# Kernel tuning notes

Measured on AMD Instinct MI355X. Metric: run time of the kernel, lower is better.

## Reference

```python
import jax, jax.numpy as jnp
import numpy as np

DIM = 2048
H = 16       # num_heads
HKV = 4      # num_kv_heads
HD = DIM // H  # head_dim = 128
REP = H // HKV
ROPE_BASE = 10000.0
QK_GAIN_INIT = 1.0
B, T = 4, 2048


def rms_norm(x):
    # F.rms_norm with eps=None -> machine eps of dtype, no weight
    eps = jnp.finfo(x.dtype).eps
    return x * jax.lax.rsqrt(jnp.mean(x * x, axis=-1, keepdims=True) + eps)


def apply_rotary_emb(x, cos, sin):
    # x: [B, h, T, HD]; cos/sin: [T, HD//2]
    h = x.shape[-1] // 2
    x1, x2 = x[..., :h], x[..., h:]
    return jnp.concatenate((x1 * cos + x2 * sin, -x1 * sin + x2 * cos), axis=-1)


def setup_inputs() -> dict:
    key = jax.random.key(0)
    ks = jax.random.split(key, 6)
    kv_dim = HKV * HD
    x = jax.random.normal(ks[0], (B, T, DIM), dtype=jnp.float32)
    Wq = jax.random.normal(ks[1], (DIM, DIM), dtype=jnp.float32) * 0.02
    Wk = jax.random.normal(ks[2], (kv_dim, DIM), dtype=jnp.float32) * 0.02
    Wv = jax.random.normal(ks[3], (kv_dim, DIM), dtype=jnp.float32) * 0.02
    Wproj = jax.random.normal(ks[4], (DIM, DIM), dtype=jnp.float32) * 0.02
    q_gain = jnp.full((H,), QK_GAIN_INIT, dtype=jnp.float32)
    return {"x": x, "Wq": Wq, "Wk": Wk, "Wv": Wv, "Wproj": Wproj, "q_gain": q_gain}


def reference(x, Wq, Wk, Wv, Wproj, q_gain):
    Bs, Ts, D = x.shape
    # QKV projections (bias-free Linear: x @ W.T)
    q = (x @ Wq.T).reshape(Bs, Ts, H, HD).transpose(0, 2, 1, 3)      # [B,H,T,HD]
    k = (x @ Wk.T).reshape(Bs, Ts, HKV, HD).transpose(0, 2, 1, 3)    # [B,HKV,T,HD]
    v = (x @ Wv.T).reshape(Bs, Ts, HKV, HD).transpose(0, 2, 1, 3)
    # RMSNorm over head_dim
    q, k = rms_norm(q), rms_norm(k)
    # rotary
    inv_freq = 1.0 / (ROPE_BASE ** (jnp.arange(0, HD, 2, dtype=jnp.float32) / HD))
    t = jnp.arange(Ts, dtype=jnp.float32)
    freqs = jnp.outer(t, inv_freq)  # [T, HD//2]
    cos, sin = jnp.cos(freqs), jnp.sin(freqs)
    q = apply_rotary_emb(q, cos, sin)
    k = apply_rotary_emb(k, cos, sin)
    # per-head query gain
    q = q * q_gain[None, :, None, None]
    # GQA attention without materializing repeated K/V
    qg = q.reshape(Bs, HKV, REP, Ts, HD)
    scale = 1.0 / jnp.sqrt(jnp.asarray(HD, dtype=q.dtype))
    scores = jnp.einsum('bgrtd,bgsd->bgrts', qg, k) * scale  # [B,HKV,REP,T,T]
    causal = jnp.tril(jnp.ones((Ts, Ts), dtype=bool))
    scores = jnp.where(causal, scores, jnp.finfo(scores.dtype).min)
    attn = jax.nn.softmax(scores, axis=-1)
    y = jnp.einsum('bgrts,bgsd->bgrtd', attn, v)              # [B,HKV,REP,T,HD]
    y = y.reshape(Bs, H, Ts, HD).transpose(0, 2, 1, 3).reshape(Bs, Ts, D)
    return y @ Wproj.T
```

## Files before the change

### kernel.cpp

```cpp
#include <hip/hip_runtime.h>
#include <stdint.h>

typedef unsigned short u16;
typedef __attribute__((ext_vector_type(4))) float f32x4;
typedef __attribute__((ext_vector_type(8))) __bf16 bf16x8;
typedef __attribute__((ext_vector_type(4))) u16 u16x4;
typedef __attribute__((ext_vector_type(8))) u16 u16x8;

#define T_SEQ 2048
#define NB 4
#define NH 16
#define NKV 4
#define HDIM 128
#define PSTR 72

__device__ __forceinline__ u16 f2bf(float f) {
  __bf16 h = (__bf16)f;
  return __builtin_bit_cast(u16, h);
}
__device__ __forceinline__ float bf2f(u16 u) {
  union { uint32_t u; float f; } v; v.u = ((uint32_t)u) << 16;
  return v.f;
}
__device__ __forceinline__ void gload16(const void* g, void* l) {
  __builtin_amdgcn_global_load_lds((const __attribute__((address_space(1))) void*)g,
                                   (__attribute__((address_space(3))) void*)l, 16, 0, 0);
}
__device__ __forceinline__ f32x4 mfma16(bf16x8 a, bf16x8 b, f32x4 c) {
  return __builtin_amdgcn_mfma_f32_16x16x32_bf16(a, b, c, 0, 0, 0);
}

__global__ __launch_bounds__(256) void cvt_all(const float* __restrict__ x,
                                               const float* __restrict__ wq,
                                               const float* __restrict__ wk,
                                               const float* __restrict__ wv,
                                               const float* __restrict__ wp,
                                               u16* __restrict__ xo, u16* __restrict__ wqo,
                                               u16* __restrict__ wko, u16* __restrict__ wvo,
                                               u16* __restrict__ wpo) {
  const int C_X = 16777216 / 4, C_WQ = 4194304 / 4, C_WKV = 1048576 / 4;
  const int B1 = C_X, B2 = B1 + C_WQ, B3 = B2 + C_WKV, B4 = B3 + C_WKV;
  const int total = B4 + C_WQ;
  int idx = blockIdx.x * 256 + threadIdx.x;
  int stride = gridDim.x * 256;
  for (int c = idx; c < total; c += stride) {
    const float* src;
    u16* dst;
    int off;
    if (c < B1)      { src = x;  dst = xo;  off = c; }
    else if (c < B2) { src = wq; dst = wqo; off = c - B1; }
    else if (c < B3) { src = wk; dst = wko; off = c - B2; }
    else if (c < B4) { src = wv; dst = wvo; off = c - B3; }
    else             { src = wp; dst = wpo; off = c - B4; }
    f32x4 v = *(const f32x4*)(src + (size_t)off * 4);
    u16x4 o;
    o[0] = f2bf(v[0]); o[1] = f2bf(v[1]); o[2] = f2bf(v[2]); o[3] = f2bf(v[3]);
    *(u16x4*)(dst + (size_t)off * 4) = o;
  }
}

template <int MODE>
__global__ __launch_bounds__(256) void gemm128p3(const u16* __restrict__ A,
                                                 const u16* __restrict__ Bt,
                                                 u16* __restrict__ k_o, u16* __restrict__ v_o,
                                                 float* __restrict__ f_o,
                                                 int K, int nx, int cpx) {
  __shared__ __align__(16) u16 As3[3 * 128 * 32];
  __shared__ __align__(16) u16 Bs3[3 * 128 * 32];
  const int tid = threadIdx.x;
  const int l = tid & 63, w = tid >> 6;
  const int l15 = l & 15, g16 = l >> 4;
  const int wr = w >> 1, wc = w & 1;

  const int oid = blockIdx.x + nx * blockIdx.y;
  const int wid = (oid & 7) * cpx + (oid >> 3);
  const int m0 = (wid / nx) * 128, n0 = (wid % nx) * 128;

  f32x4 acc[4][4] = {};

  const int row0 = tid >> 2, row1 = 64 + (tid >> 2), cc = tid & 3;
  const int sc0 = cc ^ ((row0 >> 1) & 3), sc1 = cc ^ ((row1 >> 1) & 3);
  const u16* pA0 = A + (size_t)(m0 + row0) * K + sc0 * 8;
  const u16* pA1 = A + (size_t)(m0 + row1) * K + sc1 * 8;
  const u16* pB0 = Bt + (size_t)(n0 + row0) * K + sc0 * 8;
  const u16* pB1 = Bt + (size_t)(n0 + row1) * K + sc1 * 8;

#define STAGE(buf)                                                   \
  {                                                                  \
    char* ab = (char*)As3 + (buf) * 8192 + w * 1024;                 \
    char* bb = (char*)Bs3 + (buf) * 8192 + w * 1024;                 \
    gload16(pA0, ab);                                                \
    gload16(pA1, ab + 4096);                                         \
    gload16(pB0, bb);                                                \
    gload16(pB1, bb + 4096);                                         \
    pA0 += 32; pA1 += 32; pB0 += 32; pB1 += 32;                      \
  }

#define COMPUTE(buf)                                                 \
  {                                                                  \
    const u16* AsB = As3 + (buf) * 4096;                             \
    const u16* BsB = Bs3 + (buf) * 4096;                             \
    bf16x8 af[4], bfr[4];                                            \
    _Pragma("unroll")                                                \
    for (int mt = 0; mt < 4; ++mt) {                                 \
      int arow = wr * 64 + mt * 16 + l15;                            \
      af[mt] = *(const bf16x8*)&AsB[arow * 32 +                      \
                                    ((g16 ^ ((arow >> 1) & 3)) * 8)];\
    }                                                                \
    _Pragma("unroll")                                                \
    for (int nt = 0; nt < 4; ++nt) {                                 \
      int brow = wc * 64 + nt * 16 + l15;                            \
      bfr[nt] = *(const bf16x8*)&BsB[brow * 32 +                     \
                                     ((g16 ^ ((brow >> 1) & 3)) * 8)];\
    }                                                                \
    __builtin_amdgcn_s_setprio(1);                                   \
    _Pragma("unroll")                                                \
    for (int mt = 0; mt < 4; ++mt)                                   \
      _Pragma("unroll")                                              \
      for (int nt = 0; nt < 4; ++nt)                                 \
        acc[mt][nt] = mfma16(af[mt], bfr[nt], acc[mt][nt]);          \
    __builtin_amdgcn_s_setprio(0);                                   \
  }

  const int ntiles = K >> 5;
  STAGE(0);
  STAGE(1);
  asm volatile("s_waitcnt vmcnt(4)" ::: "memory");
  __builtin_amdgcn_s_barrier();

  int cur = 0, nxt = 2;
  for (int t = 0; t < ntiles; ++t) {
    const bool more2 = (t + 2 < ntiles);
    if (more2) STAGE(nxt);
    COMPUTE(cur);
    if (t + 1 < ntiles) {
      if (more2) {
        asm volatile("s_waitcnt vmcnt(4)" ::: "memory");
      } else {
        asm volatile("s_waitcnt vmcnt(0)" ::: "memory");
      }
      __builtin_amdgcn_s_barrier();
    }
    cur = (cur == 2) ? 0 : cur + 1;
    nxt = (nxt == 2) ? 0 : nxt + 1;
  }
#undef STAGE
#undef COMPUTE

#pragma unroll
  for (int mt = 0; mt < 4; ++mt) {
#pragma unroll
    for (int r = 0; r < 4; ++r) {
      int row = m0 + wr * 64 + mt * 16 + g16 * 4 + r;
#pragma unroll
      for (int nt = 0; nt < 4; ++nt) {
        int n = n0 + wc * 64 + nt * 16 + l15;
        float val = acc[mt][nt][r];
        if (MODE == 1) {
          f_o[(size_t)row * 2048 + n] = val;
        } else {
          int b = row >> 11, t = row & (T_SEQ - 1);
          u16 bv = f2bf(val);
          if (n < 512) {
            int h = n >> 7, d = n & 127;
            k_o[((size_t)(b * NKV + h) * T_SEQ + t) * HDIM + d] = bv;
          } else {
            int n2 = n - 512; int h = n2 >> 7, d = n2 & 127;
            v_o[((size_t)(b * NKV + h) * T_SEQ + t) * HDIM + d] = bv;
          }
        }
      }
    }
  }
}

template <int MODE>
__global__ __launch_bounds__(512, 2) void gemm256(const u16* __restrict__ A,
                                                  const u16* __restrict__ Bt,
                                                  u16* __restrict__ q_o,
                                                  float* __restrict__ f_o,
                                                  int K, int ntn, int cpx) {
  __shared__ __align__(16) u16 As[2][256 * 64];
  __shared__ __align__(16) u16 Bs[2][256 * 64];
  const int tid = threadIdx.x;
  const int l = tid & 63, w = tid >> 6;
  const int l16 = l & 15, g16 = l >> 4;
  const int wr = w >> 2, wc = w & 3;

  const int oid = blockIdx.x;
  const int wid = (oid & 7) * cpx + (oid >> 3);
  const int m0 = (wid / ntn) * 256, n0 = (wid % ntn) * 256;

  f32x4 acc[8][4] = {};

  const int srow = tid >> 3, scc = tid & 7;
  const u16* pA[4];
  const u16* pB[4];
#pragma unroll
  for (int j = 0; j < 4; ++j) {
    int row = j * 64 + srow;
    int cc = scc ^ (row & 7);
    pA[j] = A + (size_t)(m0 + row) * K + cc * 8;
    pB[j] = Bt + (size_t)(n0 + row) * K + cc * 8;
  }

#define STAGE(buf)                                              \
  {                                                             \
    char* ab = (char*)As[buf] + w * 1024;                       \
    char* bb = (char*)Bs[buf] + w * 1024;                       \
    _Pragma("unroll")                                           \
    for (int j = 0; j < 4; ++j) {                               \
      gload16(pA[j], ab + j * 8192);                            \
      pA[j] += 64;                                              \
    }                                                           \
    _Pragma("unroll")                                           \
    for (int j = 0; j < 4; ++j) {                               \
      gload16(pB[j], bb + j * 8192);                            \
      pB[j] += 64;                                              \
    }                                                           \
  }

  const int ntk = K >> 6;
  STAGE(0);
  __syncthreads();

  for (int t = 0; t < ntk; ++t) {
    const int buf = t & 1;
    if (t + 1 < ntk) STAGE(buf ^ 1);
#pragma unroll
    for (int ks = 0; ks < 2; ++ks) {
      bf16x8 bfr[4];
#pragma unroll
      for (int nf = 0; nf < 4; ++nf) {
        int brow = wc * 64 + nf * 16 + l16;
        int slot = (ks * 4 + g16) ^ (brow & 7);
        bfr[nf] = *(const bf16x8*)&Bs[buf][brow * 64 + slot * 8];
      }
#pragma unroll
      for (int rh = 0; rh < 2; ++rh) {
        bf16x8 af[4];
#pragma unroll
        for (int f = 0; f < 4; ++f) {
          int arow = wr * 128 + rh * 64 + f * 16 + l16;
          int slot = (ks * 4 + g16) ^ (arow & 7);
          af[f] = *(const bf16x8*)&As[buf][arow * 64 + slot * 8];
        }
        __builtin_amdgcn_s_setprio(1);
#pragma unroll
        for (int f = 0; f < 4; ++f)
#pragma unroll
          for (int nf = 0; nf < 4; ++nf)
            acc[rh * 4 + f][nf] = mfma16(af[f], bfr[nf], acc[rh * 4 + f][nf]);
        __builtin_amdgcn_s_setprio(0);
      }
    }
    __syncthreads();
  }
#undef STAGE

#pragma unroll
  for (int rf = 0; rf < 8; ++rf) {
#pragma unroll
    for (int rr = 0; rr < 4; ++rr) {
      int row = m0 + wr * 128 + rf * 16 + g16 * 4 + rr;
#pragma unroll
      for (int nf = 0; nf < 4; ++nf) {
        int n = n0 + wc * 64 + nf * 16 + l16;
        float val = acc[rf][nf][rr];
        if (MODE == 1) {
          f_o[(size_t)row * 2048 + n] = val;
        } else {
          int b = row >> 11, t = row & (T_SEQ - 1);
          int h = n >> 7, d = n & 127;
          q_o[((size_t)(b * NH + h) * T_SEQ + t) * HDIM + d] = f2bf(val);
        }
      }
    }
  }
}

__global__ __launch_bounds__(256) void rmsrope(u16* __restrict__ buf,
                                               const float* __restrict__ gains,
                                               int nheads, float fold, int useGain) {
  const int w = threadIdx.x >> 6, l = threadIdx.x & 63;
  const int rid = blockIdx.x * 4 + w;
  const int t = rid & (T_SEQ - 1);
  const int h = (rid >> 11) % nheads;
  u16* p = buf + (size_t)rid * HDIM;
  float x1 = bf2f(p[l]), x2 = bf2f(p[l + 64]);
  float ss = x1 * x1 + x2 * x2;
#pragma unroll
  for (int m = 32; m; m >>= 1) ss += __shfl_xor(ss, m, 64);
  float rn = rsqrtf(ss * (1.0f / 128.0f) + 1.1920928955078125e-7f);
  float g = useGain ? gains[h] * fold : fold;
  float sc = rn * g;
  float inv = exp2f(-(float)l * (13.287712379549449f / 64.0f));
  float ang = (float)t * inv;
  float s, c;
  __sincosf(ang, &s, &c);
  float o1 = (x1 * c + x2 * s) * sc;
  float o2 = (x2 * c - x1 * s) * sc;
  p[l] = f2bf(o1);
  p[l + 64] = f2bf(o2);
}

__global__ __launch_bounds__(256) void vtrans(const u16* __restrict__ in,
                                              u16* __restrict__ out) {
  __shared__ u16 tileT[64][PSTR];
  const int tid = threadIdx.x;
  const int t0 = blockIdx.x * 64, d0 = blockIdx.y * 64, bg = blockIdx.z;
  const int row = tid >> 2, c0 = (tid & 3) * 16;
  const u16* src = in + ((size_t)bg * T_SEQ + t0 + row) * HDIM + d0 + c0;
  u16x8 a = *(const u16x8*)src;
  u16x8 bb = *(const u16x8*)(src + 8);
#pragma unroll
  for (int j = 0; j < 8; ++j) {
    tileT[c0 + j][row] = a[j];
    tileT[c0 + 8 + j][row] = bb[j];
  }
  __syncthreads();
  u16* dst = out + ((size_t)bg * HDIM + d0 + row) * T_SEQ + t0 + c0;
  *(u16x8*)dst = *(const u16x8*)&tileT[row][c0];
  *(u16x8*)(dst + 8) = *(const u16x8*)&tileT[row][c0 + 8];
}

__global__ __launch_bounds__(256) void attn_fwd6(const u16* __restrict__ qb,
                                                 const u16* __restrict__ kb,
                                                 const u16* __restrict__ vtb,
                                                 u16* __restrict__ yb,
                                                 const float* __restrict__ gains) {
  __shared__ __align__(16) u16 Ks[64 * 128];
  __shared__ __align__(16) u16 Vs[128 * 64];
  __shared__ __align__(16) u16 Ps[4][32 * PSTR];

  const int tid = threadIdx.x, l = tid & 63, w = tid >> 6;
  const int l16 = l & 15, g16 = l >> 4;

  const int oid = blockIdx.x + 8 * blockIdx.y;
  const int wid = (oid & 7) * 64 + (oid >> 3);
  const int pair = wid & 7, bh = wid >> 3;
  const int b = bh >> 4, h = bh & 15, gr = h >> 2;

  const float Mh = 16.33f * fabsf(gains[h]) + 0.5f;
  const u16* kbase = kb + (size_t)(b * NKV + gr) * T_SEQ * HDIM;
  const u16* vtbase = vtb + (size_t)(b * NKV + gr) * HDIM * T_SEQ;

  bf16x8 ones;
#pragma unroll
  for (int j = 0; j < 8; ++j) ones[j] = (__bf16)1.0f;

  for (int phase = 0; phase < 2; ++phase) {
    const int qt = phase ? (15 - pair) : pair;
    const int q0 = qt * 128 + w * 32;
    const int qhi = q0 + 31;

    bf16x8 qf[2][4];
    const u16* qbase = qb + ((size_t)bh * T_SEQ + q0) * HDIM;
#pragma unroll
    for (int nf = 0; nf < 2; ++nf)
#pragma unroll
      for (int s = 0; s < 4; ++s)
        qf[nf][s] = *(const bf16x8*)(qbase + (size_t)(nf * 16 + l16) * HDIM + s * 32 + g16 * 8);

    f32x4 oacc[2][8] = {};
    f32x4 dden[2] = {};
    const int ntile = 2 * qt + 2;

    for (int kt = 0; kt < ntile; ++kt) {
#pragma unroll
      for (int r = 0; r < 4; ++r) {
        int c = r * 256 + tid;
        int row = c >> 4, c16 = c & 15;
        int sc = c16 ^ (row & 7);
        gload16(kbase + ((size_t)(kt * 64 + row)) * HDIM + sc * 8,
                (char*)Ks + (r * 256 + w * 64) * 16);
      }
#pragma unroll
      for (int r = 0; r < 4; ++r) {
        int c = r * 256 + tid;
        int row = c >> 3, c8 = c & 7;
        int sc = c8 ^ (row & 7);
        gload16(vtbase + (size_t)row * T_SEQ + kt * 64 + sc * 8,
                (char*)Vs + (r * 256 + w * 64) * 16);
      }
      __syncthreads();

      if (kt * 64 <= qhi) {
        f32x4 sacc[4][2] = {};
        __builtin_amdgcn_s_setprio(1);
#pragma unroll
        for (int mt = 0; mt < 4; ++mt) {
          int key = mt * 16 + l16;
#pragma unroll
          for (int s = 0; s < 4; ++s) {
            bf16x8 kf = *(const bf16x8*)&Ks[key * 128 + ((s * 4 + g16) ^ (key & 7)) * 8];
#pragma unroll
            for (int nf = 0; nf < 2; ++nf)
              sacc[mt][nf] = mfma16(kf, qf[nf][s], sacc[mt][nf]);
          }
        }
        __builtin_amdgcn_s_setprio(0);

        const bool diagcross = (kt * 64 + 63 > q0);
#pragma unroll
        for (int mt = 0; mt < 4; ++mt) {
          int keyb = kt * 64 + mt * 16 + g16 * 4;
#pragma unroll
          for (int nf = 0; nf < 2; ++nf) {
            u16x4 p4;
#pragma unroll
            for (int r = 0; r < 4; ++r) {
              float pv = exp2f(sacc[mt][nf][r] - Mh);
              if (diagcross && (keyb + r > q0 + nf * 16 + l16)) pv = 0.f;
              p4[r] = f2bf(pv);
            }
            *(u16x4*)&Ps[w][(nf * 16 + l16) * PSTR + mt * 16 + g16 * 4] = p4;
          }
        }

        __builtin_amdgcn_s_setprio(1);
#pragma unroll
        for (int ks = 0; ks < 2; ++ks) {
          bf16x8 pa[2];
#pragma unroll
          for (int mq = 0; mq < 2; ++mq) {
            pa[mq] = *(const bf16x8*)&Ps[w][(mq * 16 + l16) * PSTR + ks * 32 + g16 * 8];
            dden[mq] = mfma16(pa[mq], ones, dden[mq]);
          }
#pragma unroll
          for (int dt = 0; dt < 8; ++dt) {
            int d = dt * 16 + l16;
            bf16x8 vv = *(const bf16x8*)&Vs[d * 64 + (((ks * 4 + g16) ^ (d & 7)) * 8)];
#pragma unroll
            for (int mq = 0; mq < 2; ++mq)
              oacc[mq][dt] = mfma16(pa[mq], vv, oacc[mq][dt]);
          }
        }
        __builtin_amdgcn_s_setprio(0);
      }
      __syncthreads();
    }

    float rden[2][4];
#pragma unroll
    for (int mq = 0; mq < 2; ++mq)
#pragma unroll
      for (int r = 0; r < 4; ++r)
        rden[mq][r] = 1.f / dden[mq][r];

#pragma unroll
    for (int mq = 0; mq < 2; ++mq)
#pragma unroll
      for (int dt = 0; dt < 8; ++dt)
#pragma unroll
        for (int r = 0; r < 4; ++r) {
          int t = q0 + mq * 16 + g16 * 4 + r;
          int d = dt * 16 + l16;
          yb[(((size_t)b * T_SEQ + t) * NH + h) * HDIM + d] = f2bf(oacc[mq][dt][r] * rden[mq][r]);
        }
    __syncthreads();
  }
}

extern "C" void kernel_launch(void* const* d_in, const int* in_sizes, int n_in,
                              void* d_out, int out_size, void* d_ws, size_t ws_size,
                              hipStream_t stream) {
  const float* x = (const float*)d_in[0];
  const float* Wq = (const float*)d_in[1];
  const float* Wk = (const float*)d_in[2];
  const float* Wv = (const float*)d_in[3];
  const float* Wproj = (const float*)d_in[4];
  const float* qg = (const float*)d_in[5];
  float* out = (float*)d_out;

  u16* xbf = (u16*)d_ws;
  u16* Wqkv = xbf + (size_t)8192 * 2048;
  u16* Wpj = Wqkv + (size_t)3072 * 2048;
  u16* qbuf = Wpj + (size_t)2048 * 2048;
  u16* kbuf = qbuf + (size_t)8192 * 2048;
  u16* vbuf = kbuf + (size_t)2048 * 2048;
  u16* ybuf = xbf;
  u16* vtbuf = Wqkv;

  cvt_all<<<2048, 256, 0, stream>>>(x, Wq, Wk, Wv, Wproj,
                                    xbf, Wqkv, Wqkv + (size_t)2048 * 2048,
                                    Wqkv + (size_t)2560 * 2048, Wpj);

  gemm256<0><<<256, 512, 0, stream>>>(xbf, Wqkv, qbuf, nullptr, 2048, 8, 32);

  gemm128p3<2><<<dim3(8, 64), 256, 0, stream>>>(xbf, Wqkv + (size_t)2048 * 2048,
                                                kbuf, vbuf, nullptr, 2048, 8, 64);

  rmsrope<<<32768, 256, 0, stream>>>(qbuf, qg, NH,
                                     1.4426950408889634f / 11.313708498984761f, 1);
  rmsrope<<<8192, 256, 0, stream>>>(kbuf, nullptr, NKV, 1.0f, 0);
  vtrans<<<dim3(32, 2, 16), 256, 0, stream>>>(vbuf, vtbuf);

  attn_fwd6<<<dim3(8, 64), 256, 0, stream>>>(qbuf, kbuf, vtbuf, ybuf, qg);

  gemm256<1><<<256, 512, 0, stream>>>(ybuf, Wpj, nullptr, out, 2048, 8, 32);
}
```

Before: 350.5 us.

## Split attention block across 8 waves with 16 query rows each

The attention kernel now launches 512 threads per block instead of 256. Each of 8 waves handles 16 query rows instead of 32, so the K/V tile staged in shared memory is shared by twice as many waves and each thread loads half as much. This lowers per-wave register use and raises the number of waves available to hide latency. In exchange, each K/V fragment read from shared memory now feeds only one MFMA instead of two, which raises LDS traffic per flop.

```diff
diff --git a/kernel.cpp b/kernel.cpp
--- a/kernel.cpp
+++ b/kernel.cpp
@@ -324,14 +324,14 @@
   *(u16x8*)(dst + 8) = *(const u16x8*)&tileT[row][c0 + 8];
 }
 
-__global__ __launch_bounds__(256) void attn_fwd6(const u16* __restrict__ qb,
+__global__ __launch_bounds__(512) void attn_fwd7(const u16* __restrict__ qb,
                                                  const u16* __restrict__ kb,
                                                  const u16* __restrict__ vtb,
                                                  u16* __restrict__ yb,
                                                  const float* __restrict__ gains) {
   __shared__ __align__(16) u16 Ks[64 * 128];
   __shared__ __align__(16) u16 Vs[128 * 64];
-  __shared__ __align__(16) u16 Ps[4][32 * PSTR];
+  __shared__ __align__(16) u16 Ps[8][16 * PSTR];
 
   const int tid = threadIdx.x, l = tid & 63, w = tid >> 6;
   const int l16 = l & 15, g16 = l >> 4;
@@ -351,42 +351,40 @@
 
   for (int phase = 0; phase < 2; ++phase) {
     const int qt = phase ? (15 - pair) : pair;
-    const int q0 = qt * 128 + w * 32;
-    const int qhi = q0 + 31;
-
-    bf16x8 qf[2][4];
+    const int q0 = qt * 128 + w * 16;
+    const int qhi = q0 + 15;
+
+    bf16x8 qf[4];
     const u16* qbase = qb + ((size_t)bh * T_SEQ + q0) * HDIM;
 #pragma unroll
-    for (int nf = 0; nf < 2; ++nf)
-#pragma unroll
-      for (int s = 0; s < 4; ++s)
-        qf[nf][s] = *(const bf16x8*)(qbase + (size_t)(nf * 16 + l16) * HDIM + s * 32 + g16 * 8);
-
-    f32x4 oacc[2][8] = {};
-    f32x4 dden[2] = {};
+    for (int s = 0; s < 4; ++s)
+      qf[s] = *(const bf16x8*)(qbase + (size_t)l16 * HDIM + s * 32 + g16 * 8);
+
+    f32x4 oacc[8] = {};
+    f32x4 dden = {};
     const int ntile = 2 * qt + 2;
 
     for (int kt = 0; kt < ntile; ++kt) {
 #pragma unroll
-      for (int r = 0; r < 4; ++r) {
-        int c = r * 256 + tid;
+      for (int r = 0; r < 2; ++r) {
+        int c = r * 512 + tid;
         int row = c >> 4, c16 = c & 15;
         int sc = c16 ^ (row & 7);
         gload16(kbase + ((size_t)(kt * 64 + row)) * HDIM + sc * 8,
-                (char*)Ks + (r * 256 + w * 64) * 16);
-      }
-#pragma unroll
-      for (int r = 0; r < 4; ++r) {
-        int c = r * 256 + tid;
+                (char*)Ks + (r * 512 + w * 64) * 16);
+      }
+#pragma unroll
+      for (int r = 0; r < 2; ++r) {
+        int c = r * 512 + tid;
         int row = c >> 3, c8 = c & 7;
         int sc = c8 ^ (row & 7);
         gload16(vtbase + (size_t)row * T_SEQ + kt * 64 + sc * 8,
-                (char*)Vs + (r * 256 + w * 64) * 16);
+                (char*)Vs + (r * 512 + w * 64) * 16);
       }
       __syncthreads();
 
       if (kt * 64 <= qhi) {
-        f32x4 sacc[4][2] = {};
+        f32x4 sacc[4] = {};
         __builtin_amdgcn_s_setprio(1);
 #pragma unroll
         for (int mt = 0; mt < 4; ++mt) {
@@ -394,9 +392,7 @@
 #pragma unroll
           for (int s = 0; s < 4; ++s) {
             bf16x8 kf = *(const bf16x8*)&Ks[key * 128 + ((s * 4 + g16) ^ (key & 7)) * 8];
-#pragma unroll
-            for (int nf = 0; nf < 2; ++nf)
-              sacc[mt][nf] = mfma16(kf, qf[nf][s], sacc[mt][nf]);
+            sacc[mt] = mfma16(kf, qf[s], sacc[mt]);
           }
         }
         __builtin_amdgcn_s_setprio(0);
@@ -405,35 +401,26 @@
 #pragma unroll
         for (int mt = 0; mt < 4; ++mt) {
           int keyb = kt * 64 + mt * 16 + g16 * 4;
-#pragma unroll
-          for (int nf = 0; nf < 2; ++nf) {
-            u16x4 p4;
-#pragma unroll
-            for (int r = 0; r < 4; ++r) {
-              float pv = exp2f(sacc[mt][nf][r] - Mh);
-              if (diagcross && (keyb + r > q0 + nf * 16 + l16)) pv = 0.f;
-              p4[r] = f2bf(pv);
-            }
-            *(u16x4*)&Ps[w][(nf * 16 + l16) * PSTR + mt * 16 + g16 * 4] = p4;
+          u16x4 p4;
+#pragma unroll
+          for (int r = 0; r < 4; ++r) {
+            float pv = exp2f(sacc[mt][r] - Mh);
+            if (diagcross && (keyb + r > q0 + l16)) pv = 0.f;
+            p4[r] = f2bf(pv);
           }
+          *(u16x4*)&Ps[w][l16 * PSTR + mt * 16 + g16 * 4] = p4;
         }
 
         __builtin_amdgcn_s_setprio(1);
 #pragma unroll
         for (int ks = 0; ks < 2; ++ks) {
-          bf16x8 pa[2];
-#pragma unroll
-          for (int mq = 0; mq < 2; ++mq) {
-            pa[mq] = *(const bf16x8*)&Ps[w][(mq * 16 + l16) * PSTR + ks * 32 + g16 * 8];
-            dden[mq] = mfma16(pa[mq], ones, dden[mq]);
-          }
+          bf16x8 pa = *(const bf16x8*)&Ps[w][l16 * PSTR + ks * 32 + g16 * 8];
+          dden = mfma16(pa, ones, dden);
 #pragma unroll
           for (int dt = 0; dt < 8; ++dt) {
             int d = dt * 16 + l16;
             bf16x8 vv = *(const bf16x8*)&Vs[d * 64 + (((ks * 4 + g16) ^ (d & 7)) * 8)];
-#pragma unroll
-            for (int mq = 0; mq < 2; ++mq)
-              oacc[mq][dt] = mfma16(pa[mq], vv, oacc[mq][dt]);
+            oacc[dt] = mfma16(pa, vv, oacc[dt]);
           }
         }
         __builtin_amdgcn_s_setprio(0);
@@ -441,23 +428,18 @@
       __syncthreads();
     }
 
-    float rden[2][4];
-#pragma unroll
-    for (int mq = 0; mq < 2; ++mq)
-#pragma unroll
-      for (int r = 0; r < 4; ++r)
-        rden[mq][r] = 1.f / dden[mq][r];
-
-#pragma unroll
-    for (int mq = 0; mq < 2; ++mq)
-#pragma unroll
-      for (int dt = 0; dt < 8; ++dt)
-#pragma unroll
-        for (int r = 0; r < 4; ++r) {
-          int t = q0 + mq * 16 + g16 * 4 + r;
-          int d = dt * 16 + l16;
-          yb[(((size_t)b * T_SEQ + t) * NH + h) * HDIM + d] = f2bf(oacc[mq][dt][r] * rden[mq][r]);
-        }
+    float rden[4];
+#pragma unroll
+    for (int r = 0; r < 4; ++r) rden[r] = 1.f / dden[r];
+
+#pragma unroll
+    for (int dt = 0; dt < 8; ++dt)
+#pragma unroll
+      for (int r = 0; r < 4; ++r) {
+        int t = q0 + g16 * 4 + r;
+        int d = dt * 16 + l16;
+        yb[(((size_t)b * T_SEQ + t) * NH + h) * HDIM + d] = f2bf(oacc[dt][r] * rden[r]);
+      }
     __syncthreads();
   }
 }
@@ -496,7 +478,7 @@
   rmsrope<<<8192, 256, 0, stream>>>(kbuf, nullptr, NKV, 1.0f, 0);
   vtrans<<<dim3(32, 2, 16), 256, 0, stream>>>(vbuf, vtbuf);
 
-  attn_fwd6<<<dim3(8, 64), 256, 0, stream>>>(qbuf, kbuf, vtbuf, ybuf, qg);
+  attn_fwd7<<<dim3(8, 64), 512, 0, stream>>>(qbuf, kbuf, vtbuf, ybuf, qg);
 
   gemm256<1><<<256, 512, 0, stream>>>(ybuf, Wpj, nullptr, out, 2048, 8, 32);
 }
```

New measurement: 348.2 us. Within noise of the previous version (-0.7%).
